# Performance work log

Hardware: AMD Instinct MI355X
Metric: run time of the kernel (lower is better)

Reference implementation:

```python
import jax, jax.numpy as jnp
import numpy as np

DIM, H, KV, S, B = 2048, 16, 4, 2048, 2
HD = DIM // H
REP = H // KV
EPS = 1e-6

def rotate_half(x):
    x1, x2 = x[..., :HD // 2], x[..., HD // 2:]
    return jnp.concatenate([-x2, x1], axis=-1)

def setup_inputs() -> dict:
    key = jax.random.key(0)
    ks = jax.random.split(key, 6)
    x = jax.random.normal(ks[0], (B, S, DIM), dtype=jnp.float32)
    sc = 1.0 / np.sqrt(DIM)
    Wq = jax.random.normal(ks[1], (DIM, H * HD), dtype=jnp.float32) * sc
    Wk = jax.random.normal(ks[2], (DIM, KV * HD), dtype=jnp.float32) * sc
    Wv = jax.random.normal(ks[3], (DIM, KV * HD), dtype=jnp.float32) * sc
    Wo = jax.random.normal(ks[4], (H * HD, DIM), dtype=jnp.float32) * sc
    qg = jnp.ones((HD,), dtype=jnp.float32)
    kg = jnp.ones((HD,), dtype=jnp.float32)
    # RoPE tables (cached buffers in the torch module)
    inv_freq = 1.0 / (10000.0 ** (jnp.arange(0, HD, 2, dtype=jnp.float32) / HD))
    freqs = jnp.arange(S, dtype=jnp.float32)[:, None] * inv_freq[None, :]
    emb = jnp.concatenate([freqs, freqs], axis=-1)  # [S, HD]
    cos, sin = jnp.cos(emb), jnp.sin(emb)
    # causal additive mask [1,1,S,S]
    mask = jnp.where(jnp.tril(jnp.ones((S, S), dtype=bool)), 0.0, -1e9)[None, None].astype(jnp.float32)
    return {"x": x, "Wq": Wq, "Wk": Wk, "Wv": Wv, "Wo": Wo,
            "qg": qg, "kg": kg, "cos": cos, "sin": sin, "mask": mask}

def rmsnorm(x, g):
    rms = jnp.sqrt(jnp.mean(x * x, axis=-1, keepdims=True) + EPS)
    return g * (x / rms)

def reference(x, Wq, Wk, Wv, Wo, qg, kg, cos, sin, mask):
    Bx, Sx, _ = x.shape
    q = (x @ Wq).reshape(Bx, Sx, H, HD).transpose(0, 2, 1, 3)   # [B,H,S,HD]
    k = (x @ Wk).reshape(Bx, Sx, KV, HD).transpose(0, 2, 1, 3)  # [B,KV,S,HD]
    v = (x @ Wv).reshape(Bx, Sx, KV, HD).transpose(0, 2, 1, 3)
    q = rmsnorm(q, qg)
    k = rmsnorm(k, kg)
    c = cos[None, None, :Sx, :]
    s = sin[None, None, :Sx, :]
    q = q * c + rotate_half(q) * s
    k = k * c + rotate_half(k) * s
    k = jnp.repeat(k, REP, axis=1)  # [B,H,S,HD]
    v = jnp.repeat(v, REP, axis=1)
    scale = 1.0 / np.sqrt(HD)
    scores = jnp.einsum('bhqd,bhkd->bhqk', q, k) * scale + mask
    attn = jax.nn.softmax(scores, axis=-1)
    out = jnp.einsum('bhqk,bhkd->bhqd', attn, v)
    out = out.transpose(0, 2, 1, 3).reshape(Bx, Sx, H * HD)
    return out @ Wo
```

## Files before the change

### kernel.cpp

```cpp
#include <hip/hip_runtime.h>

typedef unsigned short u16;
typedef __attribute__((ext_vector_type(8))) short s16x8;
typedef __attribute__((ext_vector_type(4))) float f32x4;
typedef __attribute__((ext_vector_type(4))) unsigned short u16x4;

#define DIMSZ 2048
#define NH    16
#define NKV   4
#define SEQ   2048
#define BB    2
#define HD    128
#define REPF  4
#define SCALE 0.08838834764831845f

__device__ __forceinline__ u16 f2bf(float x) {
  union { float f; unsigned u; } v; v.f = x;
  unsigned r = v.u + 0x7fffu + ((v.u >> 16) & 1u);
  return (u16)(r >> 16);
}
__device__ __forceinline__ float bf2f(u16 x) {
  union { unsigned u; float f; } v; v.u = ((unsigned)x) << 16;
  return v.f;
}
__device__ __forceinline__ unsigned pack2(float a, float b) {
  union { float f; unsigned u; } x, y; x.f = a; y.f = b;
  return ((x.u + 0x8000u) >> 16) | ((y.u + 0x8000u) & 0xffff0000u);
}
__device__ __forceinline__ void gld16(const void* g, void* l) {
  __builtin_amdgcn_global_load_lds(
      (const __attribute__((address_space(1))) unsigned int*)g,
      (__attribute__((address_space(3))) unsigned int*)l, 16, 0, 0);
}

__global__ __launch_bounds__(256) void k_cvt(const float* __restrict__ x,
                                             u16* __restrict__ o) {
  int i = (blockIdx.x * 256 + threadIdx.x) * 8;
  float4 a = *(const float4*)(x + i);
  float4 b = *(const float4*)(x + i + 4);
  u16x4 p0 = { f2bf(a.x), f2bf(a.y), f2bf(a.z), f2bf(a.w) };
  u16x4 p1 = { f2bf(b.x), f2bf(b.y), f2bf(b.z), f2bf(b.w) };
  *(u16x4*)(o + i) = p0;
  *(u16x4*)(o + i + 4) = p1;
}

__global__ __launch_bounds__(256) void k_transpose(const float* __restrict__ W,
                                                   u16* __restrict__ Wt,
                                                   int K, int N) {
  __shared__ float t[32][33];
  int tx = threadIdx.x & 31, ty = threadIdx.x >> 5;
  int r0 = blockIdx.y * 32, c0 = blockIdx.x * 32;
#pragma unroll
  for (int i = 0; i < 32; i += 8)
    t[ty + i][tx] = W[(size_t)(r0 + ty + i) * N + c0 + tx];
  __syncthreads();
#pragma unroll
  for (int i = 0; i < 32; i += 8)
    Wt[(size_t)(c0 + ty + i) * K + r0 + tx] = f2bf(t[tx][ty + i]);
}

__global__ __launch_bounds__(256) void k_gemm(const u16* __restrict__ A,
                                              const u16* __restrict__ Bt,
                                              void* __restrict__ C0,
                                              void* __restrict__ C1,
                                              void* __restrict__ C2,
                                              int M, int N, int K, int mode) {
  __shared__ __align__(16) u16 shA[128 * 64];
  __shared__ __align__(16) u16 shB[128 * 64];
  const int tid = threadIdx.x;
  const int wave = tid >> 6, lane = tid & 63;
  const int l15 = lane & 15, lh = lane >> 4;
  const int m0 = blockIdx.y * 128, n0 = blockIdx.x * 128;
  const int wr = wave >> 1, wc = wave & 1;

  const int lrow = lane >> 3, lg = lane & 7;
  const int sg = (lg ^ lrow) * 8;
  const u16* gA[4]; const u16* gB[4];
  u16* lA[4]; u16* lB[4];
#pragma unroll
  for (int t = 0; t < 4; t++) {
    int row = wave * 32 + t * 8 + lrow;
    gA[t] = A + (size_t)(m0 + row) * K + sg;
    gB[t] = Bt + (size_t)(n0 + row) * K + sg;
    lA[t] = &shA[(wave * 32 + t * 8) * 64];
    lB[t] = &shB[(wave * 32 + t * 8) * 64];
  }

  f32x4 acc[4][4] = {};
  for (int k0 = 0; k0 < K; k0 += 64) {
#pragma unroll
    for (int t = 0; t < 4; t++) {
      gld16(gA[t] + k0, lA[t]);
      gld16(gB[t] + k0, lB[t]);
    }
    __syncthreads();
#pragma unroll
    for (int kf = 0; kf < 2; kf++) {
      s16x8 af[4], bfr[4];
#pragma unroll
      for (int i = 0; i < 4; i++) {
        int rowa = wr * 64 + i * 16 + l15;
        af[i] = *(const s16x8*)&shA[rowa * 64 + (((kf * 4 + lh) ^ (l15 & 7)) * 8)];
        int rowb = wc * 64 + i * 16 + l15;
        bfr[i] = *(const s16x8*)&shB[rowb * 64 + (((kf * 4 + lh) ^ (l15 & 7)) * 8)];
      }
#pragma unroll
      for (int i = 0; i < 4; i++)
#pragma unroll
        for (int j = 0; j < 4; j++)
          acc[i][j] = __builtin_amdgcn_mfma_f32_16x16x32_bf16(af[i], bfr[j], acc[i][j], 0, 0, 0);
    }
    __syncthreads();
  }

  if (mode == 1) {
    float* C = (float*)C0;
#pragma unroll
    for (int i = 0; i < 4; i++)
#pragma unroll
      for (int j = 0; j < 4; j++)
#pragma unroll
        for (int r = 0; r < 4; r++) {
          int m = m0 + wr * 64 + i * 16 + lh * 4 + r;
          int n = n0 + wc * 64 + j * 16 + l15;
          C[(size_t)m * N + n] = acc[i][j][r];
        }
  } else {
    if (n0 < 2048) {
      u16* C = (u16*)C0;
#pragma unroll
      for (int i = 0; i < 4; i++)
#pragma unroll
        for (int j = 0; j < 4; j++)
#pragma unroll
          for (int r = 0; r < 4; r++) {
            int m = m0 + wr * 64 + i * 16 + lh * 4 + r;
            int n = n0 + wc * 64 + j * 16 + l15;
            C[(size_t)m * 2048 + n] = f2bf(acc[i][j][r]);
          }
    } else if (n0 < 2560) {
      u16* C = (u16*)C1;
#pragma unroll
      for (int i = 0; i < 4; i++)
#pragma unroll
        for (int j = 0; j < 4; j++)
#pragma unroll
          for (int r = 0; r < 4; r++) {
            int m = m0 + wr * 64 + i * 16 + lh * 4 + r;
            int n = n0 - 2048 + wc * 64 + j * 16 + l15;
            C[(size_t)m * 512 + n] = f2bf(acc[i][j][r]);
          }
    } else {
      u16* C = (u16*)C2;
#pragma unroll
      for (int i = 0; i < 4; i++)
#pragma unroll
        for (int j = 0; j < 4; j++) {
          int n = n0 - 2560 + wc * 64 + j * 16 + l15;
          int kvh = n >> 7, d = n & 127;
          int m = m0 + wr * 64 + i * 16 + lh * 4;
          int b = m >> 11, s = m & 2047;
          u16x4 pk = { f2bf(acc[i][j][0]), f2bf(acc[i][j][1]),
                       f2bf(acc[i][j][2]), f2bf(acc[i][j][3]) };
          *(u16x4*)&C[(((size_t)b * NKV + kvh) * HD + d) * SEQ + s] = pk;
        }
    }
  }
}

__global__ __launch_bounds__(256) void k_normrope(u16* __restrict__ Q,
                                                  u16* __restrict__ Kb,
                                                  const float* __restrict__ qg,
                                                  const float* __restrict__ kg,
                                                  const float* __restrict__ cosT,
                                                  const float* __restrict__ sinT) {
  int wid = (blockIdx.x * 256 + threadIdx.x) >> 6;
  int lane = threadIdx.x & 63;
  const int NQR = BB * SEQ * NH;
  u16* ptr; const float* g; int s;
  if (wid < NQR) {
    ptr = Q + (size_t)wid * HD; g = qg; s = (wid / NH) % SEQ;
  } else {
    int r2 = wid - NQR;
    ptr = Kb + (size_t)r2 * HD; g = kg; s = (r2 / NKV) % SEQ;
  }
  int d = lane * 2;
  unsigned v = *(const unsigned*)(ptr + d);
  float x0 = bf2f((u16)(v & 0xffff)), x1 = bf2f((u16)(v >> 16));
  float ss = x0 * x0 + x1 * x1;
#pragma unroll
  for (int off = 32; off >= 1; off >>= 1) ss += __shfl_xor(ss, off);
  float rinv = rsqrtf(ss * (1.0f / HD) + 1e-6f);
  float2 gv = *(const float2*)&g[d];
  float n0 = x0 * rinv * gv.x, n1 = x1 * rinv * gv.y;
  float p0 = __shfl_xor(n0, 32), p1 = __shfl_xor(n1, 32);
  float r0 = (lane < 32) ? -p0 : p0;
  float r1 = (lane < 32) ? -p1 : p1;
  float2 cc = *(const float2*)&cosT[s * HD + d];
  float2 sn = *(const float2*)&sinT[s * HD + d];
  float o0 = n0 * cc.x + r0 * sn.x, o1 = n1 * cc.y + r1 * sn.y;
  *(unsigned*)(ptr + d) = (unsigned)f2bf(o0) | ((unsigned)f2bf(o1) << 16);
}

__global__ __launch_bounds__(256) void k_attn(const u16* __restrict__ Q,
                                              const u16* __restrict__ Kb,
                                              const u16* __restrict__ Vt,
                                              u16* __restrict__ O) {
  __shared__ __align__(16) u16 shK[2][64 * 128];
  __shared__ __align__(16) u16 shV[2][128 * 64];
  __shared__ __align__(16) u16 shP[4][16 * 72];
  const int tid = threadIdx.x, wave = tid >> 6, lane = tid & 63;
  const int l15 = lane & 15, lh = lane >> 4;
  const int bid = blockIdx.x;
  const int qt = 31 - (bid >> 5);
  const int bh = bid & 31, b = bh >> 4, h = bh & 15, kvh = h >> 2;
  const int q0w = qt * 64 + wave * 16;

  const u16* qbase = Q + ((size_t)((size_t)b * SEQ + q0w + l15) * NH + h) * HD;
  s16x8 qf[4];
#pragma unroll
  for (int kf = 0; kf < 4; kf++) qf[kf] = *(const s16x8*)(qbase + kf * 32 + lh * 8);

  const u16* srcK[4]; const u16* srcV[4];
  int dstK[4], dstV[4];
#pragma unroll
  for (int t = 0; t < 4; t++) {
    int rk = wave * 16 + t * 4 + (lane >> 4);
    int gk = (lane & 15) ^ (rk & 7);
    srcK[t] = Kb + ((size_t)((size_t)b * SEQ + rk) * NKV + kvh) * HD + gk * 8;
    dstK[t] = (wave * 16 + t * 4) * 128;
    int rv = wave * 32 + t * 8 + (lane >> 3);
    int gv = (lane & 7) ^ (rv & 7);
    srcV[t] = Vt + ((size_t)((size_t)b * NKV + kvh) * HD + rv) * SEQ + gv * 8;
    dstV[t] = (wave * 32 + t * 8) * 64;
  }

  f32x4 oacc[8] = {};
  float m = -3e38f, l = 0.f;
  const int nt = qt + 1;
  const float SC2 = SCALE * 1.44269504f;

#pragma unroll
  for (int t = 0; t < 4; t++) {
    gld16(srcK[t], &shK[0][dstK[t]]);
    gld16(srcV[t], &shV[0][dstV[t]]);
  }
  __syncthreads();

  int buf = 0;
  for (int kt = 0; kt < nt; kt++) {
    if (kt + 1 < nt) {
      const size_t koff = (size_t)(kt + 1) * 64;
#pragma unroll
      for (int t = 0; t < 4; t++) {
        gld16(srcK[t] + koff * (NKV * HD), &shK[buf ^ 1][dstK[t]]);
        gld16(srcV[t] + koff, &shV[buf ^ 1][dstV[t]]);
      }
    }

    f32x4 sacc[4] = {};
#pragma unroll
    for (int kf = 0; kf < 4; kf++)
#pragma unroll
      for (int nf = 0; nf < 4; nf++) {
        s16x8 kfr = *(const s16x8*)&shK[buf][(nf * 16 + l15) * 128 + (((kf * 4 + lh) ^ (l15 & 7)) * 8)];
        sacc[nf] = __builtin_amdgcn_mfma_f32_16x16x32_bf16(kfr, qf[kf], sacc[nf], 0, 0, 0);
      }

    const int q = q0w + l15;
    float p[4][4];
    float mx = -3e38f;
    if (kt == nt - 1) {
#pragma unroll
      for (int nf = 0; nf < 4; nf++)
#pragma unroll
        for (int r = 0; r < 4; r++) {
          int k = kt * 64 + nf * 16 + lh * 4 + r;
          float s = (k <= q) ? sacc[nf][r] * SC2 : -3e38f;
          p[nf][r] = s; mx = fmaxf(mx, s);
        }
    } else {
#pragma unroll
      for (int nf = 0; nf < 4; nf++)
#pragma unroll
        for (int r = 0; r < 4; r++) {
          float s = sacc[nf][r] * SC2;
          p[nf][r] = s; mx = fmaxf(mx, s);
        }
    }
    mx = fmaxf(mx, __shfl_xor(mx, 16));
    mx = fmaxf(mx, __shfl_xor(mx, 32));

    if (!__all(mx - m <= 8.0f)) {
      float mnew = fmaxf(m, mx);
      float alpha = exp2f(m - mnew);
      l *= alpha; m = mnew;
#pragma unroll
      for (int r = 0; r < 4; r++) {
        float ar = __shfl(alpha, (lh << 2) | r);
#pragma unroll
        for (int nf = 0; nf < 8; nf++) oacc[nf][r] *= ar;
      }
    }

    float rs = 0.f;
#pragma unroll
    for (int nf = 0; nf < 4; nf++)
#pragma unroll
      for (int r = 0; r < 4; r++) {
        float pe = exp2f(p[nf][r] - m);
        p[nf][r] = pe; rs += pe;
      }
    rs += __shfl_xor(rs, 16);
    rs += __shfl_xor(rs, 32);
    l += rs;

    u16* pw = &shP[wave][l15 * 72];
#pragma unroll
    for (int nf = 0; nf < 4; nf++) {
      uint2 w2 = { pack2(p[nf][0], p[nf][1]), pack2(p[nf][2], p[nf][3]) };
      *(uint2*)(pw + nf * 16 + lh * 4) = w2;
    }
    asm volatile("s_waitcnt lgkmcnt(0)" ::: "memory");
    __builtin_amdgcn_sched_barrier(0);

#pragma unroll
    for (int kvf = 0; kvf < 2; kvf++) {
      s16x8 pf = *(const s16x8*)&shP[wave][l15 * 72 + kvf * 32 + lh * 8];
#pragma unroll
      for (int nf = 0; nf < 8; nf++) {
        s16x8 vf = *(const s16x8*)&shV[buf][(nf * 16 + l15) * 64 + (((kvf * 4 + lh) ^ (l15 & 7)) * 8)];
        oacc[nf] = __builtin_amdgcn_mfma_f32_16x16x32_bf16(pf, vf, oacc[nf], 0, 0, 0);
      }
    }
    __syncthreads();
    buf ^= 1;
  }

#pragma unroll
  for (int r = 0; r < 4; r++) {
    float lv = __shfl(l, (lh << 2) | r);
    float linv = 1.0f / lv;
    int s = q0w + lh * 4 + r;
    u16* orow = O + ((size_t)((size_t)b * SEQ + s) * NH + h) * HD;
#pragma unroll
    for (int nf = 0; nf < 8; nf++)
      orow[nf * 16 + l15] = f2bf(oacc[nf][r] * linv);
  }
}

extern "C" void kernel_launch(void* const* d_in, const int* in_sizes, int n_in,
                              void* d_out, int out_size, void* d_ws, size_t ws_size,
                              hipStream_t stream) {
  const float* x    = (const float*)d_in[0];
  const float* Wq   = (const float*)d_in[1];
  const float* Wk   = (const float*)d_in[2];
  const float* Wv   = (const float*)d_in[3];
  const float* Wo   = (const float*)d_in[4];
  const float* qg   = (const float*)d_in[5];
  const float* kg   = (const float*)d_in[6];
  const float* cosT = (const float*)d_in[7];
  const float* sinT = (const float*)d_in[8];

  char* ws = (char*)d_ws;
  const size_t MB = 1024 * 1024;
  u16* xb    = (u16*)(ws);
  u16* Wqkvt = (u16*)(ws + 16 * MB);
  u16* Wot   = (u16*)(ws + 28 * MB);
  u16* Qb    = (u16*)(ws + 36 * MB);
  u16* Kbf   = (u16*)(ws + 52 * MB);
  u16* Vt    = (u16*)(ws + 56 * MB);
  u16* Ob    = xb;

  k_cvt<<<4096, 256, 0, stream>>>(x, xb);
  k_transpose<<<dim3(DIMSZ / 32, DIMSZ / 32), 256, 0, stream>>>(Wq, Wqkvt, DIMSZ, DIMSZ);
  k_transpose<<<dim3(512 / 32, DIMSZ / 32), 256, 0, stream>>>(Wk, Wqkvt + (size_t)2048 * 2048, DIMSZ, 512);
  k_transpose<<<dim3(512 / 32, DIMSZ / 32), 256, 0, stream>>>(Wv, Wqkvt + (size_t)2560 * 2048, DIMSZ, 512);
  k_transpose<<<dim3(DIMSZ / 32, DIMSZ / 32), 256, 0, stream>>>(Wo, Wot, DIMSZ, DIMSZ);

  k_gemm<<<dim3(24, 32), 256, 0, stream>>>(xb, Wqkvt, Qb, Kbf, Vt,
                                           BB * SEQ, 3072, DIMSZ, 3);

  k_normrope<<<20480, 256, 0, stream>>>(Qb, Kbf, qg, kg, cosT, sinT);
  k_attn<<<1024, 256, 0, stream>>>(Qb, Kbf, Vt, Ob);

  k_gemm<<<dim3(16, 32), 256, 0, stream>>>(Ob, Wot, (float*)d_out, nullptr, nullptr,
                                           BB * SEQ, DIMSZ, DIMSZ, 1);
}
```

Before: 352.0 us.

## Use 256x256 double-buffered GEMM and 128-query attention blocks with priority hints

Replaces the 128x128 GEMM with a 256x256-tile, 512-thread kernel. It double-buffers LDS and interleaves the staging of the next k-tile with MFMA phases, using explicit barriers and setprio. The attention kernel now handles 128 queries per block with 8 waves, so each K/V tile load is shared by more queries, and it also raises wave priority around the MFMA sections. The aim is more data reuse and better overlap of memory with compute. The cost is fewer blocks for the GEMMs (192 and 128 tiles), which may underfill the 256 CUs, and heavier LDS and register use.

New measurement: 367.5 us. 4.4% more time.

```diff
diff --git a/kernel.cpp b/kernel.cpp
--- a/kernel.cpp
+++ b/kernel.cpp
@@ -32,6 +32,11 @@
       (const __attribute__((address_space(1))) unsigned int*)g,
       (__attribute__((address_space(3))) unsigned int*)l, 16, 0, 0);
 }
+
+#define BARX __builtin_amdgcn_s_barrier()
+#define LG0  do { asm volatile("s_waitcnt lgkmcnt(0)" ::: "memory"); \
+                  __builtin_amdgcn_sched_barrier(0); } while (0)
+#define VMW(n) asm volatile("s_waitcnt vmcnt(" #n ")" ::: "memory")
 
 __global__ __launch_bounds__(256) void k_cvt(const float* __restrict__ x,
                                              u16* __restrict__ o) {
@@ -59,109 +64,162 @@
     Wt[(size_t)(c0 + ty + i) * K + r0 + tx] = f2bf(t[tx][ty + i]);
 }
 
-__global__ __launch_bounds__(256) void k_gemm(const u16* __restrict__ A,
-                                              const u16* __restrict__ Bt,
-                                              void* __restrict__ C0,
-                                              void* __restrict__ C1,
-                                              void* __restrict__ C2,
-                                              int M, int N, int K, int mode) {
-  __shared__ __align__(16) u16 shA[128 * 64];
-  __shared__ __align__(16) u16 shB[128 * 64];
+__global__ __launch_bounds__(512, 2) void k_gemm256(const u16* __restrict__ A,
+                                                    const u16* __restrict__ Bt,
+                                                    void* __restrict__ C0,
+                                                    void* __restrict__ C1,
+                                                    void* __restrict__ C2,
+                                                    int M, int N, int K, int mode) {
+  __shared__ __align__(16) u16 shA[2][256 * 64];
+  __shared__ __align__(16) u16 shB[2][256 * 64];
   const int tid = threadIdx.x;
   const int wave = tid >> 6, lane = tid & 63;
   const int l15 = lane & 15, lh = lane >> 4;
-  const int m0 = blockIdx.y * 128, n0 = blockIdx.x * 128;
-  const int wr = wave >> 1, wc = wave & 1;
-
-  const int lrow = lane >> 3, lg = lane & 7;
-  const int sg = (lg ^ lrow) * 8;
-  const u16* gA[4]; const u16* gB[4];
-  u16* lA[4]; u16* lB[4];
-#pragma unroll
-  for (int t = 0; t < 4; t++) {
-    int row = wave * 32 + t * 8 + lrow;
-    gA[t] = A + (size_t)(m0 + row) * K + sg;
-    gB[t] = Bt + (size_t)(n0 + row) * K + sg;
-    lA[t] = &shA[(wave * 32 + t * 8) * 64];
-    lB[t] = &shB[(wave * 32 + t * 8) * 64];
-  }
-
-  f32x4 acc[4][4] = {};
-  for (int k0 = 0; k0 < K; k0 += 64) {
-#pragma unroll
-    for (int t = 0; t < 4; t++) {
-      gld16(gA[t] + k0, lA[t]);
-      gld16(gB[t] + k0, lB[t]);
-    }
-    __syncthreads();
-#pragma unroll
-    for (int kf = 0; kf < 2; kf++) {
-      s16x8 af[4], bfr[4];
-#pragma unroll
-      for (int i = 0; i < 4; i++) {
-        int rowa = wr * 64 + i * 16 + l15;
-        af[i] = *(const s16x8*)&shA[rowa * 64 + (((kf * 4 + lh) ^ (l15 & 7)) * 8)];
-        int rowb = wc * 64 + i * 16 + l15;
-        bfr[i] = *(const s16x8*)&shB[rowb * 64 + (((kf * 4 + lh) ^ (l15 & 7)) * 8)];
-      }
-#pragma unroll
-      for (int i = 0; i < 4; i++)
-#pragma unroll
-        for (int j = 0; j < 4; j++)
-          acc[i][j] = __builtin_amdgcn_mfma_f32_16x16x32_bf16(af[i], bfr[j], acc[i][j], 0, 0, 0);
-    }
-    __syncthreads();
+  const int wm = wave >> 2, wn = wave & 3;
+  const int m0 = blockIdx.y * 256, n0 = blockIdx.x * 256;
+
+  const int srow = wave * 8 + (lane >> 3);
+  const int sgr = ((lane & 7) ^ ((lane >> 3) & 7)) * 8;
+  const u16* gA = A + (size_t)(m0 + srow) * K + sgr;
+  const u16* gB = Bt + (size_t)(n0 + srow) * K + sgr;
+
+  auto stgA = [&](int rb, int kt, int sl) {
+    gld16(gA + (size_t)rb * 64 * K + (size_t)kt * 64, &shA[sl][rb * 4096 + wave * 512]);
+  };
+  auto stgB = [&](int rb, int kt, int sl) {
+    gld16(gB + (size_t)rb * 64 * K + (size_t)kt * 64, &shB[sl][rb * 4096 + wave * 512]);
+  };
+  auto rdA = [&](int mf, int ks, int sl) -> s16x8 {
+    int rl = wm * 128 + mf * 16 + l15;
+    return *(const s16x8*)&shA[sl][rl * 64 + (((ks * 4 + lh) ^ (l15 & 7)) * 8)];
+  };
+  auto rdB = [&](int nf, int ks, int sl) -> s16x8 {
+    int rl = wn * 64 + nf * 16 + l15;
+    return *(const s16x8*)&shB[sl][rl * 64 + (((ks * 4 + lh) ^ (l15 & 7)) * 8)];
+  };
+
+  f32x4 acc[8][4] = {};
+  s16x8 afr[4], bfr[4];
+  const int NK = K >> 6;
+
+  stgB(0, 0, 0); stgB(1, 0, 0); stgB(2, 0, 0); stgB(3, 0, 0);
+  stgA(0, 0, 0); stgA(2, 0, 0); stgA(1, 0, 0); stgA(3, 0, 0);
+  VMW(2);
+  BARX;
+
+  for (int t = 0; t < NK; ++t) {
+    const int sl = t & 1, ns = sl ^ 1;
+    const bool st = (t + 1 < NK);
+    const int kn = t + 1;
+
+#pragma unroll
+    for (int nf = 0; nf < 4; nf++) bfr[nf] = rdB(nf, 0, sl);
+#pragma unroll
+    for (int i = 0; i < 4; i++) afr[i] = rdA(i, 0, sl);
+    if (st) { stgB(0, kn, ns); stgB(1, kn, ns); }
+    BARX; LG0;
+    __builtin_amdgcn_s_setprio(1);
+#pragma unroll
+    for (int i = 0; i < 4; i++)
+#pragma unroll
+      for (int nf = 0; nf < 4; nf++)
+        acc[i][nf] = __builtin_amdgcn_mfma_f32_16x16x32_bf16(afr[i], bfr[nf], acc[i][nf], 0, 0, 0);
+    __builtin_amdgcn_s_setprio(0);
+    if (st) VMW(2); else VMW(0);
+    BARX;
+
+#pragma unroll
+    for (int i = 0; i < 4; i++) afr[i] = rdA(4 + i, 0, sl);
+    if (st) { stgB(2, kn, ns); stgB(3, kn, ns); }
+    BARX; LG0;
+    __builtin_amdgcn_s_setprio(1);
+#pragma unroll
+    for (int i = 0; i < 4; i++)
+#pragma unroll
+      for (int nf = 0; nf < 4; nf++)
+        acc[4 + i][nf] = __builtin_amdgcn_mfma_f32_16x16x32_bf16(afr[i], bfr[nf], acc[4 + i][nf], 0, 0, 0);
+    __builtin_amdgcn_s_setprio(0);
+    BARX;
+
+#pragma unroll
+    for (int nf = 0; nf < 4; nf++) bfr[nf] = rdB(nf, 1, sl);
+#pragma unroll
+    for (int i = 0; i < 4; i++) afr[i] = rdA(i, 1, sl);
+    if (st) { stgA(0, kn, ns); stgA(2, kn, ns); }
+    BARX; LG0;
+    __builtin_amdgcn_s_setprio(1);
+#pragma unroll
+    for (int i = 0; i < 4; i++)
+#pragma unroll
+      for (int nf = 0; nf < 4; nf++)
+        acc[i][nf] = __builtin_amdgcn_mfma_f32_16x16x32_bf16(afr[i], bfr[nf], acc[i][nf], 0, 0, 0);
+    __builtin_amdgcn_s_setprio(0);
+    BARX;
+
+#pragma unroll
+    for (int i = 0; i < 4; i++) afr[i] = rdA(4 + i, 1, sl);
+    if (st) { stgA(1, kn, ns); stgA(3, kn, ns); }
+    BARX; LG0;
+    __builtin_amdgcn_s_setprio(1);
+#pragma unroll
+    for (int i = 0; i < 4; i++)
+#pragma unroll
+      for (int nf = 0; nf < 4; nf++)
+        acc[4 + i][nf] = __builtin_amdgcn_mfma_f32_16x16x32_bf16(afr[i], bfr[nf], acc[4 + i][nf], 0, 0, 0);
+    __builtin_amdgcn_s_setprio(0);
+    if (st) VMW(2);
+    BARX;
   }
 
   if (mode == 1) {
     float* C = (float*)C0;
 #pragma unroll
-    for (int i = 0; i < 4; i++)
-#pragma unroll
-      for (int j = 0; j < 4; j++)
+    for (int mf = 0; mf < 8; mf++)
+#pragma unroll
+      for (int nf = 0; nf < 4; nf++)
 #pragma unroll
         for (int r = 0; r < 4; r++) {
-          int m = m0 + wr * 64 + i * 16 + lh * 4 + r;
-          int n = n0 + wc * 64 + j * 16 + l15;
-          C[(size_t)m * N + n] = acc[i][j][r];
+          int m = m0 + wm * 128 + mf * 16 + lh * 4 + r;
+          int n = n0 + wn * 64 + nf * 16 + l15;
+          C[(size_t)m * N + n] = acc[mf][nf][r];
         }
   } else {
     if (n0 < 2048) {
       u16* C = (u16*)C0;
 #pragma unroll
-      for (int i = 0; i < 4; i++)
-#pragma unroll
-        for (int j = 0; j < 4; j++)
+      for (int mf = 0; mf < 8; mf++)
+#pragma unroll
+        for (int nf = 0; nf < 4; nf++)
 #pragma unroll
           for (int r = 0; r < 4; r++) {
-            int m = m0 + wr * 64 + i * 16 + lh * 4 + r;
-            int n = n0 + wc * 64 + j * 16 + l15;
-            C[(size_t)m * 2048 + n] = f2bf(acc[i][j][r]);
+            int m = m0 + wm * 128 + mf * 16 + lh * 4 + r;
+            int n = n0 + wn * 64 + nf * 16 + l15;
+            C[(size_t)m * 2048 + n] = f2bf(acc[mf][nf][r]);
           }
     } else if (n0 < 2560) {
       u16* C = (u16*)C1;
 #pragma unroll
-      for (int i = 0; i < 4; i++)
-#pragma unroll
-        for (int j = 0; j < 4; j++)
+      for (int mf = 0; mf < 8; mf++)
+#pragma unroll
+        for (int nf = 0; nf < 4; nf++)
 #pragma unroll
           for (int r = 0; r < 4; r++) {
-            int m = m0 + wr * 64 + i * 16 + lh * 4 + r;
-            int n = n0 - 2048 + wc * 64 + j * 16 + l15;
-            C[(size_t)m * 512 + n] = f2bf(acc[i][j][r]);
+            int m = m0 + wm * 128 + mf * 16 + lh * 4 + r;
+            int n = n0 - 2048 + wn * 64 + nf * 16 + l15;
+            C[(size_t)m * 512 + n] = f2bf(acc[mf][nf][r]);
           }
     } else {
       u16* C = (u16*)C2;
 #pragma unroll
-      for (int i = 0; i < 4; i++)
-#pragma unroll
-        for (int j = 0; j < 4; j++) {
-          int n = n0 - 2560 + wc * 64 + j * 16 + l15;
+      for (int mf = 0; mf < 8; mf++)
+#pragma unroll
+        for (int nf = 0; nf < 4; nf++) {
+          int n = n0 - 2560 + wn * 64 + nf * 16 + l15;
           int kvh = n >> 7, d = n & 127;
-          int m = m0 + wr * 64 + i * 16 + lh * 4;
+          int m = m0 + wm * 128 + mf * 16 + lh * 4;
           int b = m >> 11, s = m & 2047;
-          u16x4 pk = { f2bf(acc[i][j][0]), f2bf(acc[i][j][1]),
-                       f2bf(acc[i][j][2]), f2bf(acc[i][j][3]) };
+          u16x4 pk = { f2bf(acc[mf][nf][0]), f2bf(acc[mf][nf][1]),
+                       f2bf(acc[mf][nf][2]), f2bf(acc[mf][nf][3]) };
           *(u16x4*)&C[(((size_t)b * NKV + kvh) * HD + d) * SEQ + s] = pk;
         }
     }
@@ -202,48 +260,49 @@
   *(unsigned*)(ptr + d) = (unsigned)f2bf(o0) | ((unsigned)f2bf(o1) << 16);
 }
 
-__global__ __launch_bounds__(256) void k_attn(const u16* __restrict__ Q,
-                                              const u16* __restrict__ Kb,
-                                              const u16* __restrict__ Vt,
-                                              u16* __restrict__ O) {
+__global__ __launch_bounds__(512, 2) void k_attn(const u16* __restrict__ Q,
+                                                 const u16* __restrict__ Kb,
+                                                 const u16* __restrict__ Vt,
+                                                 u16* __restrict__ O) {
   __shared__ __align__(16) u16 shK[2][64 * 128];
   __shared__ __align__(16) u16 shV[2][128 * 64];
-  __shared__ __align__(16) u16 shP[4][16 * 72];
+  __shared__ __align__(16) u16 shP[8][16 * 72];
   const int tid = threadIdx.x, wave = tid >> 6, lane = tid & 63;
   const int l15 = lane & 15, lh = lane >> 4;
   const int bid = blockIdx.x;
-  const int qt = 31 - (bid >> 5);
+  const int qt = 15 - (bid >> 5);
   const int bh = bid & 31, b = bh >> 4, h = bh & 15, kvh = h >> 2;
-  const int q0w = qt * 64 + wave * 16;
+  const int q0w = qt * 128 + wave * 16;
 
   const u16* qbase = Q + ((size_t)((size_t)b * SEQ + q0w + l15) * NH + h) * HD;
   s16x8 qf[4];
 #pragma unroll
   for (int kf = 0; kf < 4; kf++) qf[kf] = *(const s16x8*)(qbase + kf * 32 + lh * 8);
 
-  const u16* srcK[4]; const u16* srcV[4];
-  int dstK[4], dstV[4];
-#pragma unroll
-  for (int t = 0; t < 4; t++) {
-    int rk = wave * 16 + t * 4 + (lane >> 4);
+  const u16* srcK[2]; const u16* srcV[2];
+  int dstK[2], dstV[2];
+#pragma unroll
+  for (int c = 0; c < 2; c++) {
+    int rk = c * 32 + wave * 4 + (lane >> 4);
     int gk = (lane & 15) ^ (rk & 7);
-    srcK[t] = Kb + ((size_t)((size_t)b * SEQ + rk) * NKV + kvh) * HD + gk * 8;
-    dstK[t] = (wave * 16 + t * 4) * 128;
-    int rv = wave * 32 + t * 8 + (lane >> 3);
+    srcK[c] = Kb + ((size_t)((size_t)b * SEQ + rk) * NKV + kvh) * HD + gk * 8;
+    dstK[c] = (c * 32 + wave * 4) * 128;
+    int rv = c * 64 + wave * 8 + (lane >> 3);
     int gv = (lane & 7) ^ (rv & 7);
-    srcV[t] = Vt + ((size_t)((size_t)b * NKV + kvh) * HD + rv) * SEQ + gv * 8;
-    dstV[t] = (wave * 32 + t * 8) * 64;
+    srcV[c] = Vt + ((size_t)((size_t)b * NKV + kvh) * HD + rv) * SEQ + gv * 8;
+    dstV[c] = (c * 64 + wave * 8) * 64;
   }
 
   f32x4 oacc[8] = {};
   float m = -3e38f, l = 0.f;
-  const int nt = qt + 1;
+  const int nt = qt * 2 + 2;
+  const int tmask = q0w >> 6;
   const float SC2 = SCALE * 1.44269504f;
 
 #pragma unroll
-  for (int t = 0; t < 4; t++) {
-    gld16(srcK[t], &shK[0][dstK[t]]);
-    gld16(srcV[t], &shV[0][dstV[t]]);
+  for (int c = 0; c < 2; c++) {
+    gld16(srcK[c], &shK[0][dstK[c]]);
+    gld16(srcV[c], &shV[0][dstV[c]]);
   }
   __syncthreads();
 
@@ -252,13 +311,14 @@
     if (kt + 1 < nt) {
       const size_t koff = (size_t)(kt + 1) * 64;
 #pragma unroll
-      for (int t = 0; t < 4; t++) {
-        gld16(srcK[t] + koff * (NKV * HD), &shK[buf ^ 1][dstK[t]]);
-        gld16(srcV[t] + koff, &shV[buf ^ 1][dstV[t]]);
+      for (int c = 0; c < 2; c++) {
+        gld16(srcK[c] + koff * (NKV * HD), &shK[buf ^ 1][dstK[c]]);
+        gld16(srcV[c] + koff, &shV[buf ^ 1][dstV[c]]);
       }
     }
 
     f32x4 sacc[4] = {};
+    __builtin_amdgcn_s_setprio(1);
 #pragma unroll
     for (int kf = 0; kf < 4; kf++)
 #pragma unroll
@@ -266,11 +326,12 @@
         s16x8 kfr = *(const s16x8*)&shK[buf][(nf * 16 + l15) * 128 + (((kf * 4 + lh) ^ (l15 & 7)) * 8)];
         sacc[nf] = __builtin_amdgcn_mfma_f32_16x16x32_bf16(kfr, qf[kf], sacc[nf], 0, 0, 0);
       }
+    __builtin_amdgcn_s_setprio(0);
 
     const int q = q0w + l15;
     float p[4][4];
     float mx = -3e38f;
-    if (kt == nt - 1) {
+    if (kt >= tmask) {
 #pragma unroll
       for (int nf = 0; nf < 4; nf++)
 #pragma unroll
@@ -321,9 +382,9 @@
       uint2 w2 = { pack2(p[nf][0], p[nf][1]), pack2(p[nf][2], p[nf][3]) };
       *(uint2*)(pw + nf * 16 + lh * 4) = w2;
     }
-    asm volatile("s_waitcnt lgkmcnt(0)" ::: "memory");
-    __builtin_amdgcn_sched_barrier(0);
-
+    LG0;
+
+    __builtin_amdgcn_s_setprio(1);
 #pragma unroll
     for (int kvf = 0; kvf < 2; kvf++) {
       s16x8 pf = *(const s16x8*)&shP[wave][l15 * 72 + kvf * 32 + lh * 8];
@@ -333,6 +394,7 @@
         oacc[nf] = __builtin_amdgcn_mfma_f32_16x16x32_bf16(pf, vf, oacc[nf], 0, 0, 0);
       }
     }
+    __builtin_amdgcn_s_setprio(0);
     __syncthreads();
     buf ^= 1;
   }
@@ -378,12 +440,12 @@
   k_transpose<<<dim3(512 / 32, DIMSZ / 32), 256, 0, stream>>>(Wv, Wqkvt + (size_t)2560 * 2048, DIMSZ, 512);
   k_transpose<<<dim3(DIMSZ / 32, DIMSZ / 32), 256, 0, stream>>>(Wo, Wot, DIMSZ, DIMSZ);
 
-  k_gemm<<<dim3(24, 32), 256, 0, stream>>>(xb, Wqkvt, Qb, Kbf, Vt,
-                                           BB * SEQ, 3072, DIMSZ, 3);
+  k_gemm256<<<dim3(12, 16), 512, 0, stream>>>(xb, Wqkvt, Qb, Kbf, Vt,
+                                              BB * SEQ, 3072, DIMSZ, 3);
 
   k_normrope<<<20480, 256, 0, stream>>>(Qb, Kbf, qg, kg, cosT, sinT);
-  k_attn<<<1024, 256, 0, stream>>>(Qb, Kbf, Vt, Ob);
-
-  k_gemm<<<dim3(16, 32), 256, 0, stream>>>(Ob, Wot, (float*)d_out, nullptr, nullptr,
-                                           BB * SEQ, DIMSZ, DIMSZ, 1);
-}
+  k_attn<<<512, 512, 0, stream>>>(Qb, Kbf, Vt, Ob);
+
+  k_gemm256<<<dim3(8, 16), 512, 0, stream>>>(Ob, Wot, (float*)d_out, nullptr, nullptr,
+                                             BB * SEQ, DIMSZ, DIMSZ, 1);
+}
```
